# Kernel optimization log

Measured on AMD Instinct MI355X. Metric: run time of the kernel, lower is better.

## Reference

```python
import jax, jax.numpy as jnp
import numpy as np

EMBED = 1024
HEADS = 16
HEAD_DIM = EMBED // HEADS


def setup_inputs() -> dict:
    key = jax.random.key(0)
    k1, k2, k3, k4, k5 = jax.random.split(key, 5)
    B, S, E = 4, 2048, EMBED
    scale = 1.0 / np.sqrt(E)
    return {
        "tensor": jax.random.normal(k1, (B, S, E), dtype=jnp.float32),
        "in_proj_w": jax.random.normal(k2, (3 * E, E), dtype=jnp.float32) * scale,
        "in_proj_b": jax.random.normal(k3, (3 * E,), dtype=jnp.float32) * 0.02,
        "out_proj_w": jax.random.normal(k4, (E, E), dtype=jnp.float32) * scale,
        "out_proj_b": jax.random.normal(k5, (E,), dtype=jnp.float32) * 0.02,
        "causal_mask": 1,
    }


def reference(tensor, in_proj_w, in_proj_b, out_proj_w, out_proj_b, causal_mask):
    B, S, E = tensor.shape
    H, D = HEADS, HEAD_DIM
    # fused qkv projection (torch Linear: x @ W.T + b)
    qkv = tensor @ in_proj_w.T + in_proj_b  # [B, S, 3E]
    q, k, v = jnp.split(qkv, 3, axis=-1)
    # [B, S, E] -> [B, H, S, D]
    q = q.reshape(B, S, H, D).transpose(0, 2, 1, 3)
    k = k.reshape(B, S, H, D).transpose(0, 2, 1, 3)
    v = v.reshape(B, S, H, D).transpose(0, 2, 1, 3)
    scores = jnp.einsum("bhqd,bhkd->bhqk", q, k)  # [B, H, S, S]
    if causal_mask:
        mask = jnp.triu(jnp.ones((S, S), dtype=bool), k=1)
        scores = jnp.where(mask, -jnp.inf, scores)
    scores = scores / np.sqrt(D).astype(np.float32)
    attn = jax.nn.softmax(scores, axis=-1)
    out = jnp.einsum("bhqk,bhkd->bhqd", attn, v)  # [B, H, S, D]
    out = out.transpose(0, 2, 1, 3).reshape(B, S, E)
    return out @ out_proj_w.T + out_proj_b
```

## Files before the change

### kernel.cpp

```cpp
#include <hip/hip_runtime.h>
#include <hip/hip_bf16.h>

#define B_  4
#define S_  2048
#define E_  1024
#define H_  16
#define D_  64
#define M_  (B_*S_)
#define N3_ (3*E_)

typedef __bf16 bf16;
typedef bf16  bf16x4 __attribute__((ext_vector_type(4)));
typedef bf16  bf16x8 __attribute__((ext_vector_type(8)));
typedef float f32x4  __attribute__((ext_vector_type(4)));

#define SC2 0.18033688011112043f

__device__ __forceinline__ f32x4 mfma16(bf16x8 a, bf16x8 b, f32x4 c) {
    return __builtin_amdgcn_mfma_f32_16x16x32_bf16(a, b, c, 0, 0, 0);
}

typedef const __attribute__((address_space(1))) void* gas_t;
typedef __attribute__((address_space(3))) void* las_t;
__device__ __forceinline__ void gl_lds16(const void* g, void* l) {
    __builtin_amdgcn_global_load_lds((gas_t)g, (las_t)l, 16, 0, 0);
}

__global__ __launch_bounds__(256) void cvt_all(const float* __restrict__ x,
                                               const float* __restrict__ w_in,
                                               const float* __restrict__ w_out,
                                               bf16* __restrict__ Xbf,
                                               bf16* __restrict__ Wqkv,
                                               bf16* __restrict__ Wo) {
    const int n1 = M_ * E_ / 4, n2 = N3_ * E_ / 4, n3 = E_ * E_ / 4;
    int i = blockIdx.x * blockDim.x + threadIdx.x;
    const float* src; bf16* dst; int j;
    if (i < n1)           { src = x;     dst = Xbf;  j = i; }
    else if (i < n1 + n2) { src = w_in;  dst = Wqkv; j = i - n1; }
    else if (i < n1 + n2 + n3) { src = w_out; dst = Wo; j = i - n1 - n2; }
    else return;
    float4 v = *(const float4*)(src + (size_t)j * 4);
    bf16x4 o;
    o[0] = (bf16)v.x; o[1] = (bf16)v.y; o[2] = (bf16)v.z; o[3] = (bf16)v.w;
    *(bf16x4*)(dst + (size_t)j * 4) = o;
}

__global__ __launch_bounds__(256) void gemm_qkv(const bf16* __restrict__ X,
                                                const bf16* __restrict__ W,
                                                const float* __restrict__ bias,
                                                bf16* __restrict__ QKV) {
    __shared__ __align__(16) bf16 As[128 * 64];
    __shared__ __align__(16) bf16 Bs[128 * 64];
    const int t = threadIdx.x;
    const int wav = t >> 6, lane = t & 63, quad = lane >> 4, l15 = lane & 15;
    const int m0 = blockIdx.y * 128, n0 = blockIdx.x * 128;
    const int wr = (wav >> 1) * 64, wc = (wav & 1) * 64;
    const int srow = t >> 3;
    const int swz  = ((t & 7) ^ (srow & 7)) * 8;

    const bf16* Ablk = X + (size_t)m0 * E_;
    const bf16* Bblk = W + (size_t)n0 * E_;
    f32x4 acc[4][4] = {};

    for (int kk = 0; kk < E_; kk += 64) {
        __syncthreads();
        #pragma unroll
        for (int ps = 0; ps < 4; ++ps) {
            gl_lds16(Ablk + (size_t)(srow + ps * 32) * E_ + kk + swz, As + (size_t)(t + ps * 256) * 8);
            gl_lds16(Bblk + (size_t)(srow + ps * 32) * E_ + kk + swz, Bs + (size_t)(t + ps * 256) * 8);
        }
        __syncthreads();
        #pragma unroll
        for (int ks = 0; ks < 2; ++ks) {
            bf16x8 af[4], bw[4];
            #pragma unroll
            for (int i = 0; i < 4; ++i) {
                const int ra = wr + i * 16 + l15;
                const int rb = wc + i * 16 + l15;
                const int cx = ((ks * 4 + quad) ^ (l15 & 7)) * 8;
                af[i] = *(const bf16x8*)&As[ra * 64 + cx];
                bw[i] = *(const bf16x8*)&Bs[rb * 64 + cx];
            }
            #pragma unroll
            for (int i = 0; i < 4; ++i)
                #pragma unroll
                for (int j = 0; j < 4; ++j)
                    acc[i][j] = mfma16(af[i], bw[j], acc[i][j]);
        }
    }
    #pragma unroll
    for (int i = 0; i < 4; ++i)
        #pragma unroll
        for (int j = 0; j < 4; ++j)
            #pragma unroll
            for (int r = 0; r < 4; ++r) {
                int mg = m0 + wr + i * 16 + quad * 4 + r;
                int ng = n0 + wc + j * 16 + l15;
                float v = acc[i][j][r] + bias[ng];
                int which = ng >> 10, rem = ng & 1023;
                if (which == 0) v *= SC2;
                int h = rem >> 6, d = rem & 63;
                int b = mg >> 11, s = mg & 2047;
                QKV[(size_t)which * (B_ * H_ * S_ * D_) +
                    (((size_t)(b * H_ + h) * S_ + s) * D_ + d)] = (bf16)v;
            }
}

__global__ __launch_bounds__(256) void transposeV(const bf16* __restrict__ V,
                                                  bf16* __restrict__ Vt) {
    __shared__ __align__(16) bf16 Ts[64][72];
    const int t = threadIdx.x;
    const int bh = blockIdx.y;
    const int s0 = blockIdx.x * 64;
    const int r = t >> 2, c0 = (t & 3) * 16;
    const bf16* src = V + ((size_t)bh * S_ + s0 + r) * D_ + c0;
    *(bf16x8*)&Ts[r][c0]     = *(const bf16x8*)src;
    *(bf16x8*)&Ts[r][c0 + 8] = *(const bf16x8*)(src + 8);
    __syncthreads();
    bf16x8 o0, o1;
    #pragma unroll
    for (int e = 0; e < 8; ++e) o0[e] = Ts[c0 + e][r];
    #pragma unroll
    for (int e = 0; e < 8; ++e) o1[e] = Ts[c0 + 8 + e][r];
    bf16* dst = Vt + ((size_t)bh * D_ + r) * S_ + s0 + c0;
    *(bf16x8*)dst       = o0;
    *(bf16x8*)(dst + 8) = o1;
}

#define LDP 72

__global__ __launch_bounds__(256, 4) void attn4(const bf16* __restrict__ Q,
                                                const bf16* __restrict__ K,
                                                const bf16* __restrict__ Vt,
                                                bf16* __restrict__ O) {
    __shared__ __align__(16) bf16 Ks[64 * 64];
    __shared__ __align__(16) bf16 Vs[64 * 64];
    __shared__ __align__(16) bf16 Ps[4][16 * LDP];

    const int t = threadIdx.x;
    const int wav = t >> 6, lane = t & 63, quad = lane >> 4, l15 = lane & 15;
    const int p  = blockIdx.x >> 6;
    const int bh = blockIdx.x & 63;

    const bf16* Qb = Q  + (size_t)bh * S_ * D_;
    const bf16* Kb = K  + (size_t)bh * S_ * D_;
    const bf16* Vb = Vt + (size_t)bh * (size_t)D_ * S_;

    const int srow = t >> 3;
    const int swz  = ((t & 7) ^ (srow & 7)) * 8;
    bf16* ldsK0 = Ks + (size_t)t * 8;
    bf16* ldsK1 = Ks + (size_t)(t + 256) * 8;
    bf16* ldsV0 = Vs + (size_t)t * 8;
    bf16* ldsV1 = Vs + (size_t)(t + 256) * 8;
    bf16* Pw = &Ps[wav][0];

    const int b = bh >> 4, h = bh & 15;

    #pragma unroll 1
    for (int phase = 0; phase < 2; ++phase) {
        const int qb  = phase ? (31 - p) : p;
        const int q0w = qb * 64 + wav * 16;
        const int qg  = q0w + l15;

        bf16x8 qf0 = *(const bf16x8*)&Qb[(size_t)(q0w + l15) * D_ + quad * 8];
        bf16x8 qf1 = *(const bf16x8*)&Qb[(size_t)(q0w + l15) * D_ + 32 + quad * 8];

        f32x4 oacc[4] = {};
        float mst = -3e38f, lst = 0.f;

        const int niter = qb + 1;
        #pragma unroll 1
        for (int it = 0; it < niter; ++it) {
            const int key0 = it * 64;
            __syncthreads();
            gl_lds16(Kb + (size_t)(key0 + srow) * D_ + swz,      ldsK0);
            gl_lds16(Kb + (size_t)(key0 + srow + 32) * D_ + swz, ldsK1);
            gl_lds16(Vb + (size_t)srow * S_ + key0 + swz,        ldsV0);
            gl_lds16(Vb + (size_t)(srow + 32) * S_ + key0 + swz, ldsV1);
            __syncthreads();

            f32x4 sacc[4];
            #pragma unroll
            for (int mt = 0; mt < 4; ++mt) {
                const int krow = mt * 16 + l15;
                const int sw = krow & 7;
                bf16x8 kf0 = *(const bf16x8*)&Ks[krow * 64 + ((quad ^ sw) * 8)];
                bf16x8 kf1 = *(const bf16x8*)&Ks[krow * 64 + (((4 + quad) ^ sw) * 8)];
                f32x4 a = {};
                a = mfma16(kf0, qf0, a);
                a = mfma16(kf1, qf1, a);
                sacc[mt] = a;
            }

            float rmax = -3e38f;
            #pragma unroll
            for (int mt = 0; mt < 4; ++mt) {
                if (key0 + mt * 16 + 15 <= q0w) {
                    #pragma unroll
                    for (int r = 0; r < 4; ++r) rmax = fmaxf(rmax, sacc[mt][r]);
                } else {
                    #pragma unroll
                    for (int r = 0; r < 4; ++r) {
                        int key = key0 + mt * 16 + quad * 4 + r;
                        float v = (key > qg) ? -3e38f : sacc[mt][r];
                        sacc[mt][r] = v;
                        rmax = fmaxf(rmax, v);
                    }
                }
            }
            rmax = fmaxf(rmax, __shfl_xor(rmax, 16));
            rmax = fmaxf(rmax, __shfl_xor(rmax, 32));

            const float mn = fmaxf(mst, rmax);
            const float al = __builtin_amdgcn_exp2f(mst - mn);
            float rsum = 0.f;
            #pragma unroll
            for (int mt = 0; mt < 4; ++mt)
                #pragma unroll
                for (int r = 0; r < 4; ++r) {
                    float pv = __builtin_amdgcn_exp2f(sacc[mt][r] - mn);
                    sacc[mt][r] = pv;
                    rsum += pv;
                }
            rsum += __shfl_xor(rsum, 16);
            rsum += __shfl_xor(rsum, 32);
            lst = lst * al + rsum;
            mst = mn;

            #pragma unroll
            for (int mt = 0; mt < 4; ++mt) {
                bf16x4 pk;
                #pragma unroll
                for (int r = 0; r < 4; ++r) pk[r] = (bf16)sacc[mt][r];
                *(bf16x4*)&Pw[l15 * LDP + mt * 16 + quad * 4] = pk;
            }

            if (__ballot(al < 1.0f) != 0ull) {
                #pragma unroll
                for (int rr = 0; rr < 4; ++rr) {
                    float alr = __shfl(al, quad * 4 + rr);
                    #pragma unroll
                    for (int nt = 0; nt < 4; ++nt) oacc[nt][rr] *= alr;
                }
            }

            bf16x8 pf0 = *(const bf16x8*)&Pw[l15 * LDP + quad * 8];
            bf16x8 pf1 = *(const bf16x8*)&Pw[l15 * LDP + 32 + quad * 8];
            #pragma unroll
            for (int nt = 0; nt < 4; ++nt) {
                const int vrow = nt * 16 + l15;
                const int sw = vrow & 7;
                bf16x8 vf0 = *(const bf16x8*)&Vs[vrow * 64 + ((quad ^ sw) * 8)];
                bf16x8 vf1 = *(const bf16x8*)&Vs[vrow * 64 + (((4 + quad) ^ sw) * 8)];
                oacc[nt] = mfma16(pf0, vf0, oacc[nt]);
                oacc[nt] = mfma16(pf1, vf1, oacc[nt]);
            }
        }

        const float linv = 1.0f / lst;
        #pragma unroll
        for (int rr = 0; rr < 4; ++rr) {
            float li = __shfl(linv, quad * 4 + rr);
            const int q = q0w + quad * 4 + rr;
            #pragma unroll
            for (int nt = 0; nt < 4; ++nt)
                O[((size_t)b * S_ + q) * E_ + h * D_ + nt * 16 + l15] =
                    (bf16)(oacc[nt][rr] * li);
        }
    }
}

__global__ __launch_bounds__(256) void gemm_out(const bf16* __restrict__ A,
                                                const bf16* __restrict__ W,
                                                const float* __restrict__ bias,
                                                float* __restrict__ out) {
    __shared__ __align__(16) bf16 As[128 * 64];
    __shared__ __align__(16) bf16 Bs[128 * 64];
    const int t = threadIdx.x;
    const int wav = t >> 6, lane = t & 63, quad = lane >> 4, l15 = lane & 15;
    const int m0 = blockIdx.y * 128, n0 = blockIdx.x * 128;
    const int wr = (wav >> 1) * 64, wc = (wav & 1) * 64;
    const int srow = t >> 3;
    const int swz  = ((t & 7) ^ (srow & 7)) * 8;

    const bf16* Ablk = A + (size_t)m0 * E_;
    const bf16* Bblk = W + (size_t)n0 * E_;
    f32x4 acc[4][4] = {};

    for (int kk = 0; kk < E_; kk += 64) {
        __syncthreads();
        #pragma unroll
        for (int ps = 0; ps < 4; ++ps) {
            gl_lds16(Ablk + (size_t)(srow + ps * 32) * E_ + kk + swz, As + (size_t)(t + ps * 256) * 8);
            gl_lds16(Bblk + (size_t)(srow + ps * 32) * E_ + kk + swz, Bs + (size_t)(t + ps * 256) * 8);
        }
        __syncthreads();
        #pragma unroll
        for (int ks = 0; ks < 2; ++ks) {
            bf16x8 af[4], bw[4];
            #pragma unroll
            for (int i = 0; i < 4; ++i) {
                const int ra = wr + i * 16 + l15;
                const int rb = wc + i * 16 + l15;
                const int cx = ((ks * 4 + quad) ^ (l15 & 7)) * 8;
                af[i] = *(const bf16x8*)&As[ra * 64 + cx];
                bw[i] = *(const bf16x8*)&Bs[rb * 64 + cx];
            }
            #pragma unroll
            for (int i = 0; i < 4; ++i)
                #pragma unroll
                for (int j = 0; j < 4; ++j)
                    acc[i][j] = mfma16(af[i], bw[j], acc[i][j]);
        }
    }
    #pragma unroll
    for (int i = 0; i < 4; ++i)
        #pragma unroll
        for (int j = 0; j < 4; ++j)
            #pragma unroll
            for (int r = 0; r < 4; ++r) {
                int mg = m0 + wr + i * 16 + quad * 4 + r;
                int ng = n0 + wc + j * 16 + l15;
                out[(size_t)mg * E_ + ng] = acc[i][j][r] + bias[ng];
            }
}

extern "C" void kernel_launch(void* const* d_in, const int* in_sizes, int n_in,
                              void* d_out, int out_size, void* d_ws, size_t ws_size,
                              hipStream_t stream) {
    const float* x     = (const float*)d_in[0];
    const float* w_in  = (const float*)d_in[1];
    const float* b_in  = (const float*)d_in[2];
    const float* w_out = (const float*)d_in[3];
    const float* b_out = (const float*)d_in[4];
    float* out = (float*)d_out;

    char* ws = (char*)d_ws;
    bf16* Xbf  = (bf16*)ws; ws += (size_t)M_ * E_ * 2;
    bf16* Wqkv = (bf16*)ws; ws += (size_t)N3_ * E_ * 2;
    bf16* Wo   = (bf16*)ws; ws += (size_t)E_ * E_ * 2;
    bf16* QKV  = (bf16*)ws; ws += (size_t)3 * B_ * H_ * S_ * D_ * 2;
    bf16* Vt   = (bf16*)ws;
    bf16* Obf  = Xbf;

    const int nCvt = (M_ * E_ + N3_ * E_ + E_ * E_) / 4;
    cvt_all<<<(nCvt + 255) / 256, 256, 0, stream>>>(x, w_in, w_out, Xbf, Wqkv, Wo);

    gemm_qkv<<<dim3(N3_ / 128, M_ / 128), 256, 0, stream>>>(Xbf, Wqkv, b_in, QKV);

    bf16* Qp = QKV;
    bf16* Kp = QKV + (size_t)B_ * H_ * S_ * D_;
    bf16* Vp = QKV + (size_t)2 * B_ * H_ * S_ * D_;

    transposeV<<<dim3(S_ / 64, B_ * H_), 256, 0, stream>>>(Vp, Vt);

    attn4<<<dim3(16 * B_ * H_), 256, 0, stream>>>(Qp, Kp, Vt, Obf);

    gemm_out<<<dim3(E_ / 128, M_ / 128), 256, 0, stream>>>(Obf, Wo, b_out, out);
}
```

Before: 265.1 us.

## Fuse V transpose into QKV GEMM epilogue and register-prefetch K/V in attention

The QKV GEMM now swaps its MFMA operands for V tiles, so each lane holds consecutive sequence positions and writes V directly in transposed layout. This removes the separate transposeV kernel and its extra read and write of V. The attention kernel replaces direct global-to-LDS loads with register staging: the next K/V tile is loaded into registers while the current one is computed, and LDS uses padded rows instead of XOR swizzle. This overlaps global latency with compute, at the cost of extra registers and LDS store instructions.

```diff
diff --git a/kernel.cpp b/kernel.cpp
--- a/kernel.cpp
+++ b/kernel.cpp
@@ -25,6 +25,8 @@
 __device__ __forceinline__ void gl_lds16(const void* g, void* l) {
     __builtin_amdgcn_global_load_lds((gas_t)g, (las_t)l, 16, 0, 0);
 }
+
+#define WAIT_LGKM0() __builtin_amdgcn_s_waitcnt(0xC07F)
 
 __global__ __launch_bounds__(256) void cvt_all(const float* __restrict__ x,
                                                const float* __restrict__ w_in,
@@ -48,7 +50,8 @@
 __global__ __launch_bounds__(256) void gemm_qkv(const bf16* __restrict__ X,
                                                 const bf16* __restrict__ W,
                                                 const float* __restrict__ bias,
-                                                bf16* __restrict__ QKV) {
+                                                bf16* __restrict__ QKV,
+                                                bf16* __restrict__ Vt) {
     __shared__ __align__(16) bf16 As[128 * 64];
     __shared__ __align__(16) bf16 Bs[128 * 64];
     const int t = threadIdx.x;
@@ -57,6 +60,7 @@
     const int wr = (wav >> 1) * 64, wc = (wav & 1) * 64;
     const int srow = t >> 3;
     const int swz  = ((t & 7) ^ (srow & 7)) * 8;
+    const bool isV = (n0 >= 2 * E_);
 
     const bf16* Ablk = X + (size_t)m0 * E_;
     const bf16* Bblk = W + (size_t)n0 * E_;
@@ -81,60 +85,65 @@
                 af[i] = *(const bf16x8*)&As[ra * 64 + cx];
                 bw[i] = *(const bf16x8*)&Bs[rb * 64 + cx];
             }
-            #pragma unroll
-            for (int i = 0; i < 4; ++i)
-                #pragma unroll
-                for (int j = 0; j < 4; ++j)
-                    acc[i][j] = mfma16(af[i], bw[j], acc[i][j]);
+            if (!isV) {
+                #pragma unroll
+                for (int i = 0; i < 4; ++i)
+                    #pragma unroll
+                    for (int j = 0; j < 4; ++j)
+                        acc[i][j] = mfma16(af[i], bw[j], acc[i][j]);
+            } else {
+                #pragma unroll
+                for (int i = 0; i < 4; ++i)
+                    #pragma unroll
+                    for (int j = 0; j < 4; ++j)
+                        acc[i][j] = mfma16(bw[i], af[j], acc[i][j]);
+            }
         }
     }
-    #pragma unroll
-    for (int i = 0; i < 4; ++i)
-        #pragma unroll
-        for (int j = 0; j < 4; ++j)
-            #pragma unroll
-            for (int r = 0; r < 4; ++r) {
-                int mg = m0 + wr + i * 16 + quad * 4 + r;
-                int ng = n0 + wc + j * 16 + l15;
-                float v = acc[i][j][r] + bias[ng];
-                int which = ng >> 10, rem = ng & 1023;
-                if (which == 0) v *= SC2;
-                int h = rem >> 6, d = rem & 63;
-                int b = mg >> 11, s = mg & 2047;
-                QKV[(size_t)which * (B_ * H_ * S_ * D_) +
-                    (((size_t)(b * H_ + h) * S_ + s) * D_ + d)] = (bf16)v;
-            }
-}
-
-__global__ __launch_bounds__(256) void transposeV(const bf16* __restrict__ V,
-                                                  bf16* __restrict__ Vt) {
-    __shared__ __align__(16) bf16 Ts[64][72];
-    const int t = threadIdx.x;
-    const int bh = blockIdx.y;
-    const int s0 = blockIdx.x * 64;
-    const int r = t >> 2, c0 = (t & 3) * 16;
-    const bf16* src = V + ((size_t)bh * S_ + s0 + r) * D_ + c0;
-    *(bf16x8*)&Ts[r][c0]     = *(const bf16x8*)src;
-    *(bf16x8*)&Ts[r][c0 + 8] = *(const bf16x8*)(src + 8);
-    __syncthreads();
-    bf16x8 o0, o1;
-    #pragma unroll
-    for (int e = 0; e < 8; ++e) o0[e] = Ts[c0 + e][r];
-    #pragma unroll
-    for (int e = 0; e < 8; ++e) o1[e] = Ts[c0 + 8 + e][r];
-    bf16* dst = Vt + ((size_t)bh * D_ + r) * S_ + s0 + c0;
-    *(bf16x8*)dst       = o0;
-    *(bf16x8*)(dst + 8) = o1;
-}
-
+    if (!isV) {
+        #pragma unroll
+        for (int i = 0; i < 4; ++i)
+            #pragma unroll
+            for (int j = 0; j < 4; ++j)
+                #pragma unroll
+                for (int r = 0; r < 4; ++r) {
+                    int mg = m0 + wr + i * 16 + quad * 4 + r;
+                    int ng = n0 + wc + j * 16 + l15;
+                    float v = acc[i][j][r] + bias[ng];
+                    int which = ng >> 10, rem = ng & 1023;
+                    if (which == 0) v *= SC2;
+                    int h = rem >> 6, d = rem & 63;
+                    int b = mg >> 11, s = mg & 2047;
+                    QKV[(size_t)which * (B_ * H_ * S_ * D_) +
+                        (((size_t)(b * H_ + h) * S_ + s) * D_ + d)] = (bf16)v;
+                }
+    } else {
+        #pragma unroll
+        for (int i = 0; i < 4; ++i)
+            #pragma unroll
+            for (int j = 0; j < 4; ++j)
+                #pragma unroll
+                for (int r = 0; r < 4; ++r) {
+                    int ng = n0 + wc + i * 16 + quad * 4 + r;
+                    int mg = m0 + wr + j * 16 + l15;
+                    float v = acc[i][j][r] + bias[ng];
+                    int rem = ng & 1023;
+                    int h = rem >> 6, d = rem & 63;
+                    int b = mg >> 11, s = mg & 2047;
+                    Vt[(((size_t)(b * H_ + h) * D_ + d) * S_) + s] = (bf16)v;
+                }
+    }
+}
+
+#define LDK 72
 #define LDP 72
 
-__global__ __launch_bounds__(256, 4) void attn4(const bf16* __restrict__ Q,
+__global__ __launch_bounds__(256, 4) void attn5(const bf16* __restrict__ Q,
                                                 const bf16* __restrict__ K,
                                                 const bf16* __restrict__ Vt,
                                                 bf16* __restrict__ O) {
-    __shared__ __align__(16) bf16 Ks[64 * 64];
-    __shared__ __align__(16) bf16 Vs[64 * 64];
+    __shared__ __align__(16) bf16 Ks[64 * LDK];
+    __shared__ __align__(16) bf16 Vs[64 * LDK];
     __shared__ __align__(16) bf16 Ps[4][16 * LDP];
 
     const int t = threadIdx.x;
@@ -146,15 +155,13 @@
     const bf16* Kb = K  + (size_t)bh * S_ * D_;
     const bf16* Vb = Vt + (size_t)bh * (size_t)D_ * S_;
 
-    const int srow = t >> 3;
-    const int swz  = ((t & 7) ^ (srow & 7)) * 8;
-    bf16* ldsK0 = Ks + (size_t)t * 8;
-    bf16* ldsK1 = Ks + (size_t)(t + 256) * 8;
-    bf16* ldsV0 = Vs + (size_t)t * 8;
-    bf16* ldsV1 = Vs + (size_t)(t + 256) * 8;
+    const int rk = t >> 2;
+    const int ck = (t & 3) * 16;
     bf16* Pw = &Ps[wav][0];
 
     const int b = bh >> 4, h = bh & 15;
+
+    bf16x8 stK0, stK1, stV0, stV1;
 
     #pragma unroll 1
     for (int phase = 0; phase < 2; ++phase) {
@@ -169,23 +176,35 @@
         float mst = -3e38f, lst = 0.f;
 
         const int niter = qb + 1;
+        stK0 = *(const bf16x8*)&Kb[(size_t)rk * D_ + ck];
+        stK1 = *(const bf16x8*)&Kb[(size_t)rk * D_ + ck + 8];
+        stV0 = *(const bf16x8*)&Vb[(size_t)rk * S_ + ck];
+        stV1 = *(const bf16x8*)&Vb[(size_t)rk * S_ + ck + 8];
+
         #pragma unroll 1
         for (int it = 0; it < niter; ++it) {
             const int key0 = it * 64;
-            __syncthreads();
-            gl_lds16(Kb + (size_t)(key0 + srow) * D_ + swz,      ldsK0);
-            gl_lds16(Kb + (size_t)(key0 + srow + 32) * D_ + swz, ldsK1);
-            gl_lds16(Vb + (size_t)srow * S_ + key0 + swz,        ldsV0);
-            gl_lds16(Vb + (size_t)(srow + 32) * S_ + key0 + swz, ldsV1);
-            __syncthreads();
+            __builtin_amdgcn_s_barrier();
+            *(bf16x8*)&Ks[rk * LDK + ck]     = stK0;
+            *(bf16x8*)&Ks[rk * LDK + ck + 8] = stK1;
+            *(bf16x8*)&Vs[rk * LDK + ck]     = stV0;
+            *(bf16x8*)&Vs[rk * LDK + ck + 8] = stV1;
+            if (it + 1 < niter) {
+                const int kn = key0 + 64;
+                stK0 = *(const bf16x8*)&Kb[(size_t)(kn + rk) * D_ + ck];
+                stK1 = *(const bf16x8*)&Kb[(size_t)(kn + rk) * D_ + ck + 8];
+                stV0 = *(const bf16x8*)&Vb[(size_t)rk * S_ + kn + ck];
+                stV1 = *(const bf16x8*)&Vb[(size_t)rk * S_ + kn + ck + 8];
+            }
+            WAIT_LGKM0();
+            __builtin_amdgcn_s_barrier();
 
             f32x4 sacc[4];
             #pragma unroll
             for (int mt = 0; mt < 4; ++mt) {
                 const int krow = mt * 16 + l15;
-                const int sw = krow & 7;
-                bf16x8 kf0 = *(const bf16x8*)&Ks[krow * 64 + ((quad ^ sw) * 8)];
-                bf16x8 kf1 = *(const bf16x8*)&Ks[krow * 64 + (((4 + quad) ^ sw) * 8)];
+                bf16x8 kf0 = *(const bf16x8*)&Ks[krow * LDK + quad * 8];
+                bf16x8 kf1 = *(const bf16x8*)&Ks[krow * LDK + 32 + quad * 8];
                 f32x4 a = {};
                 a = mfma16(kf0, qf0, a);
                 a = mfma16(kf1, qf1, a);
@@ -249,9 +268,8 @@
             #pragma unroll
             for (int nt = 0; nt < 4; ++nt) {
                 const int vrow = nt * 16 + l15;
-                const int sw = vrow & 7;
-                bf16x8 vf0 = *(const bf16x8*)&Vs[vrow * 64 + ((quad ^ sw) * 8)];
-                bf16x8 vf1 = *(const bf16x8*)&Vs[vrow * 64 + (((4 + quad) ^ sw) * 8)];
+                bf16x8 vf0 = *(const bf16x8*)&Vs[vrow * LDK + quad * 8];
+                bf16x8 vf1 = *(const bf16x8*)&Vs[vrow * LDK + 32 + quad * 8];
                 oacc[nt] = mfma16(pf0, vf0, oacc[nt]);
                 oacc[nt] = mfma16(pf1, vf1, oacc[nt]);
             }
@@ -339,22 +357,19 @@
     bf16* Xbf  = (bf16*)ws; ws += (size_t)M_ * E_ * 2;
     bf16* Wqkv = (bf16*)ws; ws += (size_t)N3_ * E_ * 2;
     bf16* Wo   = (bf16*)ws; ws += (size_t)E_ * E_ * 2;
-    bf16* QKV  = (bf16*)ws; ws += (size_t)3 * B_ * H_ * S_ * D_ * 2;
-    bf16* Vt   = (bf16*)ws;
+    bf16* QKV  = (bf16*)ws; ws += (size_t)2 * B_ * H_ * S_ * D_ * 2;
+    bf16* Vt   = (bf16*)ws; ws += (size_t)B_ * H_ * S_ * D_ * 2;
     bf16* Obf  = Xbf;
 
     const int nCvt = (M_ * E_ + N3_ * E_ + E_ * E_) / 4;
     cvt_all<<<(nCvt + 255) / 256, 256, 0, stream>>>(x, w_in, w_out, Xbf, Wqkv, Wo);
 
-    gemm_qkv<<<dim3(N3_ / 128, M_ / 128), 256, 0, stream>>>(Xbf, Wqkv, b_in, QKV);
+    gemm_qkv<<<dim3(N3_ / 128, M_ / 128), 256, 0, stream>>>(Xbf, Wqkv, b_in, QKV, Vt);
 
     bf16* Qp = QKV;
     bf16* Kp = QKV + (size_t)B_ * H_ * S_ * D_;
-    bf16* Vp = QKV + (size_t)2 * B_ * H_ * S_ * D_;
-
-    transposeV<<<dim3(S_ / 64, B_ * H_), 256, 0, stream>>>(Vp, Vt);
-
-    attn4<<<dim3(16 * B_ * H_), 256, 0, stream>>>(Qp, Kp, Vt, Obf);
+
+    attn5<<<dim3(16 * B_ * H_), 256, 0, stream>>>(Qp, Kp, Vt, Obf);
 
     gemm_out<<<dim3(E_ / 128, M_ / 128), 256, 0, stream>>>(Obf, Wo, b_out, out);
 }
```

Result: faster. 257.4 us (-2.9%).
